# Optimization experiments

Hardware: AMD Instinct MI355X
Metric: run time of the kernel (lower is better)

## Reference

```python
import jax, jax.numpy as jnp
import numpy as np

E = 16          # num_experts
F_C = 2.0       # capacity factor
D = 1024        # embed_dim
I = 4 * D       # expert intermediate (mlp_ratio * embed_dim)
IS = 2 * D      # shared-expert intermediate (num_shared_experts * embed_dim)
B, S = 4, 1024


def setup_inputs() -> dict:
    key = jax.random.key(0)
    ks = jax.random.split(key, 8)
    w = 0.02
    return {
        "hidden_states": jax.random.normal(ks[0], (B, S, D), dtype=jnp.float32),
        "gate_w": jax.random.normal(ks[1], (E, D), dtype=jnp.float32) * w,
        "Wg": jax.random.normal(ks[2], (E, I, D), dtype=jnp.float32) * w,  # gate_proj per expert
        "Wu": jax.random.normal(ks[3], (E, I, D), dtype=jnp.float32) * w,  # up_proj per expert
        "Wd": jax.random.normal(ks[4], (E, D, I), dtype=jnp.float32) * w,  # down_proj per expert
        "Sg": jax.random.normal(ks[5], (IS, D), dtype=jnp.float32) * w,    # shared gate_proj
        "Su": jax.random.normal(ks[6], (IS, D), dtype=jnp.float32) * w,    # shared up_proj
        "Sd": jax.random.normal(ks[7], (D, IS), dtype=jnp.float32) * w,    # shared down_proj
    }


def reference(hidden_states, gate_w, Wg, Wu, Wd, Sg, Su, Sd):
    b, s, d = hidden_states.shape
    T = b * s
    C = int(T * F_C / E)  # expert capacity, static
    flat_x = hidden_states.reshape(T, d)

    # --- expert-choice gating ---
    logits = flat_x @ gate_w.T                      # (T, E)
    scores = jax.nn.softmax(logits, axis=-1).T      # (E, T)
    topk_weight, topk_idx = jax.lax.top_k(scores, C)  # (E, C)

    # --- gather tokens per expert ---
    xg = flat_x[topk_idx]                           # (E, C, d)

    # --- per-expert GELU-gated MLP (batched as grouped GEMMs) ---
    g = jnp.einsum('ecd,eid->eci', xg, Wg)          # (E, C, I)
    u = jnp.einsum('ecd,eid->eci', xg, Wu)          # (E, C, I)
    h = jax.nn.gelu(g, approximate=False) * u       # exact GELU matches nn.GELU()
    eo = jnp.einsum('eci,edi->ecd', h, Wd)          # (E, C, d)
    eo = eo * topk_weight[..., None]

    # --- weighted scatter-add back to tokens ---
    flat_out = jnp.zeros_like(flat_x).at[topk_idx.reshape(-1)].add(eo.reshape(-1, d))
    out = flat_out.reshape(b, s, d)

    # --- shared experts on all tokens ---
    sg = hidden_states @ Sg.T                       # (B, S, IS)
    su = hidden_states @ Su.T
    shared = (jax.nn.gelu(sg, approximate=False) * su) @ Sd.T  # (B, S, d)
    return out + shared
```

## Files before the change

kernel.cpp:

```cpp
#include <hip/hip_runtime.h>
#include <hip/hip_bf16.h>
#include <math.h>

#define NE   16
#define DDIM 1024
#define II   4096
#define ISD  2048
#define TT   4096
#define CAP  512

typedef __attribute__((ext_vector_type(8))) short short8;
typedef __attribute__((ext_vector_type(4))) float floatx4;

static __device__ __forceinline__ unsigned short f2b(float f){
  unsigned int x = __float_as_uint(f);
  return (unsigned short)((x + 0x7fffu + ((x >> 16) & 1u)) >> 16);
}

static __device__ __forceinline__ float gelu_exact(float x){
  return 0.5f * x * (1.0f + erff(x * 0.70710678118654752f));
}

#define ASYNC_COPY16(gptr, lptr)                                                    \
  __builtin_amdgcn_global_load_lds((const __attribute__((address_space(1))) void*)(gptr), \
                                   (__attribute__((address_space(3))) void*)(lptr), \
                                   16, 0, 0)

__global__ void gating_kernel(const float* __restrict__ x, const float* __restrict__ gw,
                              float* __restrict__ scores){
  const int wave = threadIdx.x >> 6, lane = threadIdx.x & 63;
  const int t = blockIdx.x * 4 + wave;
  const float* xp = x + (size_t)t * DDIM;
  float xr[16];
  #pragma unroll
  for (int i = 0; i < 16; i++) xr[i] = xp[i * 64 + lane];
  double logit[NE];
  #pragma unroll
  for (int e = 0; e < NE; e++){
    const float* g = gw + (size_t)e * DDIM;
    double s = 0.0;
    #pragma unroll
    for (int i = 0; i < 16; i++) s += (double)xr[i] * (double)g[i * 64 + lane];
    #pragma unroll
    for (int off = 32; off > 0; off >>= 1) s += __shfl_xor(s, off);
    logit[e] = s;
  }
  double m = logit[0];
  #pragma unroll
  for (int e = 1; e < NE; e++) m = fmax(m, logit[e]);
  double p[NE], sum = 0.0;
  #pragma unroll
  for (int e = 0; e < NE; e++){ p[e] = exp(logit[e] - m); sum += p[e]; }
  if (lane == 0){
    #pragma unroll
    for (int e = 0; e < NE; e++) scores[(size_t)e * TT + t] = (float)(p[e] / sum);
  }
}

__global__ void topk_kernel(const float* __restrict__ scores, int* __restrict__ cnt,
                            int* __restrict__ tidx, float* __restrict__ tw){
  const int e = blockIdx.y;
  __shared__ float s[TT];
  const float* se = scores + (size_t)e * TT;
  for (int i = threadIdx.x; i < TT; i += 256) s[i] = se[i];
  __syncthreads();
  const int t = blockIdx.x * 256 + threadIdx.x;
  const float ms = s[t];
  int r = 0;
  const float4* s4 = reinterpret_cast<const float4*>(s);
  for (int j = 0; j < TT / 4; j++){
    float4 v = s4[j];
    int b = j * 4;
    r += (v.x > ms) || (v.x == ms && (b + 0) < t);
    r += (v.y > ms) || (v.y == ms && (b + 1) < t);
    r += (v.z > ms) || (v.z == ms && (b + 2) < t);
    r += (v.w > ms) || (v.w == ms && (b + 3) < t);
  }
  if (r < CAP){
    int p = atomicAdd(&cnt[e], 1);
    tidx[e * CAP + p] = t;
    tw[e * CAP + p]   = ms;
  }
}

__global__ void cvt_bf16_kernel(const float* __restrict__ src, unsigned short* __restrict__ dst,
                                int n4){
  int i = blockIdx.x * 256 + threadIdx.x;
  const int stride = gridDim.x * 256;
  const float4* s = reinterpret_cast<const float4*>(src);
  ushort4* d = reinterpret_cast<ushort4*>(dst);
  for (; i < n4; i += stride){
    float4 v = s[i];
    ushort4 o; o.x = f2b(v.x); o.y = f2b(v.y); o.z = f2b(v.z); o.w = f2b(v.w);
    d[i] = o;
  }
}

__global__ void gather_b16_kernel(const unsigned short* __restrict__ xb,
                                  const int* __restrict__ tidx,
                                  unsigned short* __restrict__ Xg){
  const int ec = blockIdx.x;
  const int tok = tidx[ec];
  const ushort4* src = reinterpret_cast<const ushort4*>(xb + (size_t)tok * DDIM);
  ushort4* dst = reinterpret_cast<ushort4*>(Xg + (size_t)ec * DDIM);
  dst[threadIdx.x] = src[threadIdx.x];
}

__global__ void gather_kernel(const float* __restrict__ x, const int* __restrict__ tidx,
                              unsigned short* __restrict__ Xg){
  const int ec = blockIdx.x;
  const int tok = tidx[ec];
  const float4* src = reinterpret_cast<const float4*>(x + (size_t)tok * DDIM);
  ushort4* dst = reinterpret_cast<ushort4*>(Xg + (size_t)ec * DDIM);
  float4 v = src[threadIdx.x];
  ushort4 o; o.x = f2b(v.x); o.y = f2b(v.y); o.z = f2b(v.z); o.w = f2b(v.w);
  dst[threadIdx.x] = o;
}

__launch_bounds__(256, 2)
__global__ void gateup_bf16_kernel(const unsigned short* __restrict__ A,
                                   const unsigned short* __restrict__ Bg,
                                   const unsigned short* __restrict__ Bu,
                                   unsigned short* __restrict__ Hout,
                                   int M, int N, int K, long sA, long sB, long sH){
  __shared__ __align__(16) unsigned short As[128 * 32];
  __shared__ __align__(16) unsigned short Bgs[128 * 32];
  __shared__ __align__(16) unsigned short Bus[128 * 32];
  const int tid = threadIdx.x;
  const int z = blockIdx.z;
  A  += (size_t)z * sA;  Bg += (size_t)z * sB;  Bu += (size_t)z * sB;  Hout += (size_t)z * sH;
  const int bm = blockIdx.x * 128, bn = blockIdx.y * 128;
  const int lane = tid & 63, wave = tid >> 6;
  const int wr = wave >> 1, wc = wave & 1;
  const int fr = lane & 15, fq = lane >> 4;

  const int srow = tid >> 2;
  const int scol = (tid & 3) * 8;
  const unsigned short* gA = A  + (size_t)(bm + srow) * K + scol;
  const unsigned short* gG = Bg + (size_t)(bn + srow) * K + scol;
  const unsigned short* gU = Bu + (size_t)(bn + srow) * K + scol;
  const size_t half = (size_t)64 * K;
  unsigned short* lA = As  + tid * 8;
  unsigned short* lG = Bgs + tid * 8;
  unsigned short* lU = Bus + tid * 8;

  floatx4 accG[4][4], accU[4][4];
  const floatx4 z4 = {0.f, 0.f, 0.f, 0.f};
  #pragma unroll
  for (int m = 0; m < 4; m++)
    #pragma unroll
    for (int n = 0; n < 4; n++){ accG[m][n] = z4; accU[m][n] = z4; }

  for (int k0 = 0; k0 < K; k0 += 32){
    ASYNC_COPY16(gA + k0,        lA);
    ASYNC_COPY16(gA + half + k0, lA + 2048);
    ASYNC_COPY16(gG + k0,        lG);
    ASYNC_COPY16(gG + half + k0, lG + 2048);
    ASYNC_COPY16(gU + k0,        lU);
    ASYNC_COPY16(gU + half + k0, lU + 2048);
    __syncthreads();
    short8 aF[4], gF[4], uF[4];
    #pragma unroll
    for (int m = 0; m < 4; m++)
      aF[m] = *reinterpret_cast<const short8*>(&As[(wr * 64 + m * 16 + fr) * 32 + fq * 8]);
    #pragma unroll
    for (int n = 0; n < 4; n++){
      gF[n] = *reinterpret_cast<const short8*>(&Bgs[(wc * 64 + n * 16 + fr) * 32 + fq * 8]);
      uF[n] = *reinterpret_cast<const short8*>(&Bus[(wc * 64 + n * 16 + fr) * 32 + fq * 8]);
    }
    #pragma unroll
    for (int m = 0; m < 4; m++)
      #pragma unroll
      for (int n = 0; n < 4; n++){
        accG[m][n] = __builtin_amdgcn_mfma_f32_16x16x32_bf16(aF[m], gF[n], accG[m][n], 0, 0, 0);
        accU[m][n] = __builtin_amdgcn_mfma_f32_16x16x32_bf16(aF[m], uF[n], accU[m][n], 0, 0, 0);
      }
    __syncthreads();
  }
  #pragma unroll
  for (int m = 0; m < 4; m++)
    #pragma unroll
    for (int n = 0; n < 4; n++){
      const int col  = bn + wc * 64 + n * 16 + fr;
      const int row0 = bm + wr * 64 + m * 16 + fq * 4;
      #pragma unroll
      for (int i = 0; i < 4; i++){
        float g = accG[m][n][i], u = accU[m][n][i];
        Hout[(size_t)(row0 + i) * N + col] = f2b(gelu_exact(g) * u);
      }
    }
}

template<int ATOMIC>
__launch_bounds__(256, 2)
__global__ void down_bf16_kernel(const unsigned short* __restrict__ A,
                                 const unsigned short* __restrict__ B,
                                 float* __restrict__ out,
                                 const int* __restrict__ tidx, const float* __restrict__ tw,
                                 int M, int N, int K, long sA, long sB){
  __shared__ __align__(16) unsigned short As[128 * 32];
  __shared__ __align__(16) unsigned short Bs[128 * 32];
  const int tid = threadIdx.x;
  const int z = blockIdx.z;
  A += (size_t)z * sA;  B += (size_t)z * sB;
  const int bm = blockIdx.x * 128, bn = blockIdx.y * 128;
  const int lane = tid & 63, wave = tid >> 6;
  const int wr = wave >> 1, wc = wave & 1;
  const int fr = lane & 15, fq = lane >> 4;

  const int srow = tid >> 2;
  const int scol = (tid & 3) * 8;
  const unsigned short* gA = A + (size_t)(bm + srow) * K + scol;
  const unsigned short* gB = B + (size_t)(bn + srow) * K + scol;
  const size_t half = (size_t)64 * K;
  unsigned short* lA = As + tid * 8;
  unsigned short* lB = Bs + tid * 8;

  floatx4 acc[4][4];
  const floatx4 z4 = {0.f, 0.f, 0.f, 0.f};
  #pragma unroll
  for (int m = 0; m < 4; m++)
    #pragma unroll
    for (int n = 0; n < 4; n++) acc[m][n] = z4;

  for (int k0 = 0; k0 < K; k0 += 32){
    ASYNC_COPY16(gA + k0,        lA);
    ASYNC_COPY16(gA + half + k0, lA + 2048);
    ASYNC_COPY16(gB + k0,        lB);
    ASYNC_COPY16(gB + half + k0, lB + 2048);
    __syncthreads();
    short8 aF[4], bF[4];
    #pragma unroll
    for (int m = 0; m < 4; m++)
      aF[m] = *reinterpret_cast<const short8*>(&As[(wr * 64 + m * 16 + fr) * 32 + fq * 8]);
    #pragma unroll
    for (int n = 0; n < 4; n++)
      bF[n] = *reinterpret_cast<const short8*>(&Bs[(wc * 64 + n * 16 + fr) * 32 + fq * 8]);
    #pragma unroll
    for (int m = 0; m < 4; m++)
      #pragma unroll
      for (int n = 0; n < 4; n++)
        acc[m][n] = __builtin_amdgcn_mfma_f32_16x16x32_bf16(aF[m], bF[n], acc[m][n], 0, 0, 0);
    __syncthreads();
  }
  #pragma unroll
  for (int m = 0; m < 4; m++)
    #pragma unroll
    for (int n = 0; n < 4; n++){
      const int col  = bn + wc * 64 + n * 16 + fr;
      const int row0 = bm + wr * 64 + m * 16 + fq * 4;
      #pragma unroll
      for (int i = 0; i < 4; i++){
        float val = acc[m][n][i];
        if constexpr (ATOMIC){
          const int r = row0 + i;
          const int token = tidx[z * CAP + r];
          const float wgt = tw[z * CAP + r];
          atomicAdd(&out[(size_t)token * DDIM + col], val * wgt);
        } else {
          out[(size_t)(row0 + i) * N + col] = val;
        }
      }
    }
}

#define LDT 40
template<typename TA>
__launch_bounds__(256, 2)
__global__ void gateup_kernel(const TA* __restrict__ A, const float* __restrict__ Bg,
                              const float* __restrict__ Bu, unsigned short* __restrict__ H,
                              int M, int N, int K, long sA, long sB, long sH){
  __shared__ unsigned short As[128 * LDT];
  __shared__ unsigned short Bgs[128 * LDT];
  __shared__ unsigned short Bus[128 * LDT];
  const int tid = threadIdx.x;
  const int z = blockIdx.z;
  A  += (size_t)z * sA;  Bg += (size_t)z * sB;  Bu += (size_t)z * sB;  H += (size_t)z * sH;
  const int bm = blockIdx.x * 128, bn = blockIdx.y * 128;
  const int lane = tid & 63, wave = tid >> 6;
  const int wr = wave >> 1, wc = wave & 1;
  const int fr = lane & 15, fq = lane >> 4;

  floatx4 accG[4][4], accU[4][4];
  const floatx4 z4 = {0.f, 0.f, 0.f, 0.f};
  #pragma unroll
  for (int m = 0; m < 4; m++)
    #pragma unroll
    for (int n = 0; n < 4; n++){ accG[m][n] = z4; accU[m][n] = z4; }

  for (int k0 = 0; k0 < K; k0 += 32){
    #pragma unroll
    for (int p = 0; p < 4; p++){
      const int row = p * 32 + (tid >> 3);
      const int col = (tid & 7) * 4;
      if constexpr (__is_same(TA, float)){
        float4 v = *reinterpret_cast<const float4*>(A + (size_t)(bm + row) * K + k0 + col);
        ushort4 o; o.x = f2b(v.x); o.y = f2b(v.y); o.z = f2b(v.z); o.w = f2b(v.w);
        *reinterpret_cast<ushort4*>(&As[row * LDT + col]) = o;
      } else {
        *reinterpret_cast<ushort4*>(&As[row * LDT + col]) =
            *reinterpret_cast<const ushort4*>(A + (size_t)(bm + row) * K + k0 + col);
      }
      float4 vg = *reinterpret_cast<const float4*>(Bg + (size_t)(bn + row) * K + k0 + col);
      ushort4 og; og.x = f2b(vg.x); og.y = f2b(vg.y); og.z = f2b(vg.z); og.w = f2b(vg.w);
      *reinterpret_cast<ushort4*>(&Bgs[row * LDT + col]) = og;
      float4 vu = *reinterpret_cast<const float4*>(Bu + (size_t)(bn + row) * K + k0 + col);
      ushort4 ou; ou.x = f2b(vu.x); ou.y = f2b(vu.y); ou.z = f2b(vu.z); ou.w = f2b(vu.w);
      *reinterpret_cast<ushort4*>(&Bus[row * LDT + col]) = ou;
    }
    __syncthreads();
    short8 aF[4], gF[4], uF[4];
    #pragma unroll
    for (int m = 0; m < 4; m++)
      aF[m] = *reinterpret_cast<const short8*>(&As[(wr * 64 + m * 16 + fr) * LDT + fq * 8]);
    #pragma unroll
    for (int n = 0; n < 4; n++){
      gF[n] = *reinterpret_cast<const short8*>(&Bgs[(wc * 64 + n * 16 + fr) * LDT + fq * 8]);
      uF[n] = *reinterpret_cast<const short8*>(&Bus[(wc * 64 + n * 16 + fr) * LDT + fq * 8]);
    }
    #pragma unroll
    for (int m = 0; m < 4; m++)
      #pragma unroll
      for (int n = 0; n < 4; n++){
        accG[m][n] = __builtin_amdgcn_mfma_f32_16x16x32_bf16(aF[m], gF[n], accG[m][n], 0, 0, 0);
        accU[m][n] = __builtin_amdgcn_mfma_f32_16x16x32_bf16(aF[m], uF[n], accU[m][n], 0, 0, 0);
      }
    __syncthreads();
  }
  #pragma unroll
  for (int m = 0; m < 4; m++)
    #pragma unroll
    for (int n = 0; n < 4; n++){
      const int col  = bn + wc * 64 + n * 16 + fr;
      const int row0 = bm + wr * 64 + m * 16 + fq * 4;
      #pragma unroll
      for (int i = 0; i < 4; i++){
        float g = accG[m][n][i], u = accU[m][n][i];
        H[(size_t)(row0 + i) * N + col] = f2b(gelu_exact(g) * u);
      }
    }
}

template<int ATOMIC>
__launch_bounds__(256, 2)
__global__ void down_kernel(const unsigned short* __restrict__ A, const float* __restrict__ B,
                            float* __restrict__ out, const int* __restrict__ tidx,
                            const float* __restrict__ tw,
                            int M, int N, int K, long sA, long sB){
  __shared__ unsigned short As[128 * LDT];
  __shared__ unsigned short Bs[128 * LDT];
  const int tid = threadIdx.x;
  const int z = blockIdx.z;
  A += (size_t)z * sA;  B += (size_t)z * sB;
  const int bm = blockIdx.x * 128, bn = blockIdx.y * 128;
  const int lane = tid & 63, wave = tid >> 6;
  const int wr = wave >> 1, wc = wave & 1;
  const int fr = lane & 15, fq = lane >> 4;

  floatx4 acc[4][4];
  const floatx4 z4 = {0.f, 0.f, 0.f, 0.f};
  #pragma unroll
  for (int m = 0; m < 4; m++)
    #pragma unroll
    for (int n = 0; n < 4; n++) acc[m][n] = z4;

  for (int k0 = 0; k0 < K; k0 += 32){
    #pragma unroll
    for (int p = 0; p < 4; p++){
      const int row = p * 32 + (tid >> 3);
      const int col = (tid & 7) * 4;
      *reinterpret_cast<ushort4*>(&As[row * LDT + col]) =
          *reinterpret_cast<const ushort4*>(A + (size_t)(bm + row) * K + k0 + col);
      float4 v = *reinterpret_cast<const float4*>(B + (size_t)(bn + row) * K + k0 + col);
      ushort4 o; o.x = f2b(v.x); o.y = f2b(v.y); o.z = f2b(v.z); o.w = f2b(v.w);
      *reinterpret_cast<ushort4*>(&Bs[row * LDT + col]) = o;
    }
    __syncthreads();
    short8 aF[4], bF[4];
    #pragma unroll
    for (int m = 0; m < 4; m++)
      aF[m] = *reinterpret_cast<const short8*>(&As[(wr * 64 + m * 16 + fr) * LDT + fq * 8]);
    #pragma unroll
    for (int n = 0; n < 4; n++)
      bF[n] = *reinterpret_cast<const short8*>(&Bs[(wc * 64 + n * 16 + fr) * LDT + fq * 8]);
    #pragma unroll
    for (int m = 0; m < 4; m++)
      #pragma unroll
      for (int n = 0; n < 4; n++)
        acc[m][n] = __builtin_amdgcn_mfma_f32_16x16x32_bf16(aF[m], bF[n], acc[m][n], 0, 0, 0);
    __syncthreads();
  }
  #pragma unroll
  for (int m = 0; m < 4; m++)
    #pragma unroll
    for (int n = 0; n < 4; n++){
      const int col  = bn + wc * 64 + n * 16 + fr;
      const int row0 = bm + wr * 64 + m * 16 + fq * 4;
      #pragma unroll
      for (int i = 0; i < 4; i++){
        float val = acc[m][n][i];
        if constexpr (ATOMIC){
          const int r = row0 + i;
          const int token = tidx[z * CAP + r];
          const float wgt = tw[z * CAP + r];
          atomicAdd(&out[(size_t)token * DDIM + col], val * wgt);
        } else {
          out[(size_t)(row0 + i) * N + col] = val;
        }
      }
    }
}

extern "C" void kernel_launch(void* const* d_in, const int* in_sizes, int n_in,
                              void* d_out, int out_size, void* d_ws, size_t ws_size,
                              hipStream_t stream){
  const float* x  = (const float*)d_in[0];
  const float* gw = (const float*)d_in[1];
  const float* Wg = (const float*)d_in[2];
  const float* Wu = (const float*)d_in[3];
  const float* Wd = (const float*)d_in[4];
  const float* Sg = (const float*)d_in[5];
  const float* Su = (const float*)d_in[6];
  const float* Sd = (const float*)d_in[7];
  float* out = (float*)d_out;

  char* w = (char*)d_ws;
  float* scores        = (float*)w;           w += (size_t)NE * TT * 4;
  int*   cnt           = (int*)w;             w += 256;
  int*   tidx          = (int*)w;             w += (size_t)NE * CAP * 4;
  float* tw            = (float*)w;           w += (size_t)NE * CAP * 4;
  unsigned short* Xg   = (unsigned short*)w;  w += (size_t)NE * CAP * DDIM * 2;
  unsigned short* H    = (unsigned short*)w;  w += (size_t)NE * CAP * II * 2;
  unsigned short* Hs   = (unsigned short*)w;  w += (size_t)TT * ISD * 2;

  const size_t base_used = (size_t)(w - (char*)d_ws);
  const size_t need_extra = (size_t)TT * DDIM * 2
                          + (size_t)NE * II * DDIM * 2 * 2
                          + (size_t)NE * DDIM * II * 2
                          + (size_t)ISD * DDIM * 2 * 2
                          + (size_t)DDIM * ISD * 2;
  const bool fast = (base_used + need_extra) <= ws_size;

  hipMemsetAsync(cnt, 0, NE * sizeof(int), stream);
  gating_kernel<<<TT / 4, 256, 0, stream>>>(x, gw, scores);
  topk_kernel<<<dim3(TT / 256, NE), 256, 0, stream>>>(scores, cnt, tidx, tw);

  if (fast){
    unsigned short* xb  = (unsigned short*)w;  w += (size_t)TT * DDIM * 2;
    unsigned short* bWg = (unsigned short*)w;  w += (size_t)NE * II * DDIM * 2;
    unsigned short* bWu = (unsigned short*)w;  w += (size_t)NE * II * DDIM * 2;
    unsigned short* bWd = (unsigned short*)w;  w += (size_t)NE * DDIM * II * 2;
    unsigned short* bSg = (unsigned short*)w;  w += (size_t)ISD * DDIM * 2;
    unsigned short* bSu = (unsigned short*)w;  w += (size_t)ISD * DDIM * 2;
    unsigned short* bSd = (unsigned short*)w;  w += (size_t)DDIM * ISD * 2;

    cvt_bf16_kernel<<<1024, 256, 0, stream>>>(x,  xb,  TT * DDIM / 4);
    cvt_bf16_kernel<<<2048, 256, 0, stream>>>(Wg, bWg, NE * II * DDIM / 4);
    cvt_bf16_kernel<<<2048, 256, 0, stream>>>(Wu, bWu, NE * II * DDIM / 4);
    cvt_bf16_kernel<<<2048, 256, 0, stream>>>(Wd, bWd, NE * DDIM * II / 4);
    cvt_bf16_kernel<<<512, 256, 0, stream>>>(Sg, bSg, ISD * DDIM / 4);
    cvt_bf16_kernel<<<512, 256, 0, stream>>>(Su, bSu, ISD * DDIM / 4);
    cvt_bf16_kernel<<<512, 256, 0, stream>>>(Sd, bSd, DDIM * ISD / 4);

    gather_b16_kernel<<<NE * CAP, 256, 0, stream>>>(xb, tidx, Xg);

    gateup_bf16_kernel<<<dim3(TT / 128, ISD / 128, 1), 256, 0, stream>>>(
        xb, bSg, bSu, Hs, TT, ISD, DDIM, 0, 0, 0);
    down_bf16_kernel<0><<<dim3(TT / 128, DDIM / 128, 1), 256, 0, stream>>>(
        Hs, bSd, out, nullptr, nullptr, TT, DDIM, ISD, 0, 0);

    gateup_bf16_kernel<<<dim3(CAP / 128, II / 128, NE), 256, 0, stream>>>(
        Xg, bWg, bWu, H, CAP, II, DDIM, (long)CAP * DDIM, (long)II * DDIM, (long)CAP * II);
    down_bf16_kernel<1><<<dim3(CAP / 128, DDIM / 128, NE), 256, 0, stream>>>(
        H, bWd, out, tidx, tw, CAP, DDIM, II, (long)CAP * II, (long)DDIM * II);
  } else {
    gather_kernel<<<NE * CAP, 256, 0, stream>>>(x, tidx, Xg);

    gateup_kernel<float><<<dim3(TT / 128, ISD / 128, 1), 256, 0, stream>>>(
        x, Sg, Su, Hs, TT, ISD, DDIM, 0, 0, 0);
    down_kernel<0><<<dim3(TT / 128, DDIM / 128, 1), 256, 0, stream>>>(
        Hs, Sd, out, nullptr, nullptr, TT, DDIM, ISD, 0, 0);

    gateup_kernel<unsigned short><<<dim3(CAP / 128, II / 128, NE), 256, 0, stream>>>(
        Xg, Wg, Wu, H, CAP, II, DDIM, (long)CAP * DDIM, (long)II * DDIM, (long)CAP * II);
    down_kernel<1><<<dim3(CAP / 128, DDIM / 128, NE), 256, 0, stream>>>(
        H, Wd, out, tidx, tw, CAP, DDIM, II, (long)CAP * II, (long)DDIM * II);
  }
}
```

Before: 1.380 ms.

## Double-buffer GEMM tiles, fuse fp32→bf16 down-weight conversion, flatten grid with XCD swizzle

```diff
diff --git a/kernel.cpp b/kernel.cpp
--- a/kernel.cpp
+++ b/kernel.cpp
@@ -25,6 +25,12 @@
   __builtin_amdgcn_global_load_lds((const __attribute__((address_space(1))) void*)(gptr), \
                                    (__attribute__((address_space(3))) void*)(lptr), \
                                    16, 0, 0)
+
+static __device__ __forceinline__ int xcd_swizzle(int lid, int nblk){
+  if (nblk & 7) return lid;
+  const int cpx = nblk >> 3;
+  return (lid & 7) * cpx + (lid >> 3);
+}
 
 __global__ void gating_kernel(const float* __restrict__ x, const float* __restrict__ gw,
                               float* __restrict__ scores){
@@ -118,31 +124,28 @@
 }
 
 __launch_bounds__(256, 2)
-__global__ void gateup_bf16_kernel(const unsigned short* __restrict__ A,
-                                   const unsigned short* __restrict__ Bg,
-                                   const unsigned short* __restrict__ Bu,
-                                   unsigned short* __restrict__ Hout,
-                                   int M, int N, int K, long sA, long sB, long sH){
-  __shared__ __align__(16) unsigned short As[128 * 32];
-  __shared__ __align__(16) unsigned short Bgs[128 * 32];
-  __shared__ __align__(16) unsigned short Bus[128 * 32];
+__global__ void gateup2_kernel(const unsigned short* __restrict__ A,
+                               const unsigned short* __restrict__ Bg,
+                               const unsigned short* __restrict__ Bu,
+                               unsigned short* __restrict__ Hout,
+                               int M, int N, int K, long sB, int nm){
+  __shared__ __align__(16) unsigned short As[2][128 * 32];
+  __shared__ __align__(16) unsigned short Bgs[2][128 * 32];
+  __shared__ __align__(16) unsigned short Bus[2][128 * 32];
   const int tid = threadIdx.x;
-  const int z = blockIdx.z;
-  A  += (size_t)z * sA;  Bg += (size_t)z * sB;  Bu += (size_t)z * sB;  Hout += (size_t)z * sH;
-  const int bm = blockIdx.x * 128, bn = blockIdx.y * 128;
+  const int swz = xcd_swizzle(blockIdx.x, gridDim.x);
+  const int mt = swz % nm, ntile = swz / nm;
+  const int bm = mt * 128, bn = ntile * 128;
+  Bg += (size_t)(mt >> 2) * sB;
+  Bu += (size_t)(mt >> 2) * sB;
   const int lane = tid & 63, wave = tid >> 6;
   const int wr = wave >> 1, wc = wave & 1;
   const int fr = lane & 15, fq = lane >> 4;
 
-  const int srow = tid >> 2;
-  const int scol = (tid & 3) * 8;
-  const unsigned short* gA = A  + (size_t)(bm + srow) * K + scol;
-  const unsigned short* gG = Bg + (size_t)(bn + srow) * K + scol;
-  const unsigned short* gU = Bu + (size_t)(bn + srow) * K + scol;
+  const unsigned short* gA = A  + (size_t)(bm + (tid >> 2)) * K + (tid & 3) * 8;
+  const unsigned short* gG = Bg + (size_t)(bn + (tid >> 2)) * K + (tid & 3) * 8;
+  const unsigned short* gU = Bu + (size_t)(bn + (tid >> 2)) * K + (tid & 3) * 8;
   const size_t half = (size_t)64 * K;
-  unsigned short* lA = As  + tid * 8;
-  unsigned short* lG = Bgs + tid * 8;
-  unsigned short* lU = Bus + tid * 8;
 
   floatx4 accG[4][4], accU[4][4];
   const floatx4 z4 = {0.f, 0.f, 0.f, 0.f};
@@ -151,22 +154,28 @@
     #pragma unroll
     for (int n = 0; n < 4; n++){ accG[m][n] = z4; accU[m][n] = z4; }
 
+  auto stage = [&](int b, int k0){
+    ASYNC_COPY16(gA + k0,        &As[b][tid * 8]);
+    ASYNC_COPY16(gA + half + k0, &As[b][tid * 8 + 2048]);
+    ASYNC_COPY16(gG + k0,        &Bgs[b][tid * 8]);
+    ASYNC_COPY16(gG + half + k0, &Bgs[b][tid * 8 + 2048]);
+    ASYNC_COPY16(gU + k0,        &Bus[b][tid * 8]);
+    ASYNC_COPY16(gU + half + k0, &Bus[b][tid * 8 + 2048]);
+  };
+
+  stage(0, 0);
+  __syncthreads();
+  int buf = 0;
   for (int k0 = 0; k0 < K; k0 += 32){
-    ASYNC_COPY16(gA + k0,        lA);
-    ASYNC_COPY16(gA + half + k0, lA + 2048);
-    ASYNC_COPY16(gG + k0,        lG);
-    ASYNC_COPY16(gG + half + k0, lG + 2048);
-    ASYNC_COPY16(gU + k0,        lU);
-    ASYNC_COPY16(gU + half + k0, lU + 2048);
-    __syncthreads();
+    if (k0 + 32 < K) stage(buf ^ 1, k0 + 32);
     short8 aF[4], gF[4], uF[4];
     #pragma unroll
     for (int m = 0; m < 4; m++)
-      aF[m] = *reinterpret_cast<const short8*>(&As[(wr * 64 + m * 16 + fr) * 32 + fq * 8]);
+      aF[m] = *reinterpret_cast<const short8*>(&As[buf][(wr * 64 + m * 16 + fr) * 32 + fq * 8]);
     #pragma unroll
     for (int n = 0; n < 4; n++){
-      gF[n] = *reinterpret_cast<const short8*>(&Bgs[(wc * 64 + n * 16 + fr) * 32 + fq * 8]);
-      uF[n] = *reinterpret_cast<const short8*>(&Bus[(wc * 64 + n * 16 + fr) * 32 + fq * 8]);
+      gF[n] = *reinterpret_cast<const short8*>(&Bgs[buf][(wc * 64 + n * 16 + fr) * 32 + fq * 8]);
+      uF[n] = *reinterpret_cast<const short8*>(&Bus[buf][(wc * 64 + n * 16 + fr) * 32 + fq * 8]);
     }
     #pragma unroll
     for (int m = 0; m < 4; m++)
@@ -176,6 +185,7 @@
         accU[m][n] = __builtin_amdgcn_mfma_f32_16x16x32_bf16(aF[m], uF[n], accU[m][n], 0, 0, 0);
       }
     __syncthreads();
+    buf ^= 1;
   }
   #pragma unroll
   for (int m = 0; m < 4; m++)
@@ -193,28 +203,24 @@
 
 template<int ATOMIC>
 __launch_bounds__(256, 2)
-__global__ void down_bf16_kernel(const unsigned short* __restrict__ A,
-                                 const unsigned short* __restrict__ B,
-                                 float* __restrict__ out,
-                                 const int* __restrict__ tidx, const float* __restrict__ tw,
-                                 int M, int N, int K, long sA, long sB){
-  __shared__ __align__(16) unsigned short As[128 * 32];
-  __shared__ __align__(16) unsigned short Bs[128 * 32];
+__global__ void down2_kernel(const unsigned short* __restrict__ A, const float* __restrict__ B,
+                             float* __restrict__ out, const int* __restrict__ tidx,
+                             const float* __restrict__ tw,
+                             int M, int N, int K, long sB, int nm){
+  __shared__ __align__(16) unsigned short As[2][128 * 32];
+  __shared__ __align__(16) unsigned short Bs[2][128 * 32];
   const int tid = threadIdx.x;
-  const int z = blockIdx.z;
-  A += (size_t)z * sA;  B += (size_t)z * sB;
-  const int bm = blockIdx.x * 128, bn = blockIdx.y * 128;
+  const int swz = xcd_swizzle(blockIdx.x, gridDim.x);
+  const int mt = swz % nm, ntile = swz / nm;
+  const int bm = mt * 128, bn = ntile * 128;
+  B += (size_t)(mt >> 2) * sB;
   const int lane = tid & 63, wave = tid >> 6;
   const int wr = wave >> 1, wc = wave & 1;
   const int fr = lane & 15, fq = lane >> 4;
 
-  const int srow = tid >> 2;
-  const int scol = (tid & 3) * 8;
-  const unsigned short* gA = A + (size_t)(bm + srow) * K + scol;
-  const unsigned short* gB = B + (size_t)(bn + srow) * K + scol;
+  const unsigned short* gA = A + (size_t)(bm + (tid >> 2)) * K + (tid & 3) * 8;
+  const float* gB = B + (size_t)bn * K;
   const size_t half = (size_t)64 * K;
-  unsigned short* lA = As + tid * 8;
-  unsigned short* lB = Bs + tid * 8;
 
   floatx4 acc[4][4];
   const floatx4 z4 = {0.f, 0.f, 0.f, 0.f};
@@ -223,25 +229,40 @@
     #pragma unroll
     for (int n = 0; n < 4; n++) acc[m][n] = z4;
 
+  auto stageA = [&](int b, int k0){
+    ASYNC_COPY16(gA + k0,        &As[b][tid * 8]);
+    ASYNC_COPY16(gA + half + k0, &As[b][tid * 8 + 2048]);
+  };
+  auto stageB = [&](int b, int k0){
+    #pragma unroll
+    for (int p = 0; p < 4; p++){
+      const int row = p * 32 + (tid >> 3);
+      const int col = (tid & 7) * 4;
+      float4 v = *reinterpret_cast<const float4*>(gB + (size_t)row * K + k0 + col);
+      ushort4 o; o.x = f2b(v.x); o.y = f2b(v.y); o.z = f2b(v.z); o.w = f2b(v.w);
+      *reinterpret_cast<ushort4*>(&Bs[b][row * 32 + col]) = o;
+    }
+  };
+
+  stageA(0, 0); stageB(0, 0);
+  __syncthreads();
+  int buf = 0;
   for (int k0 = 0; k0 < K; k0 += 32){
-    ASYNC_COPY16(gA + k0,        lA);
-    ASYNC_COPY16(gA + half + k0, lA + 2048);
-    ASYNC_COPY16(gB + k0,        lB);
-    ASYNC_COPY16(gB + half + k0, lB + 2048);
-    __syncthreads();
+    if (k0 + 32 < K){ stageA(buf ^ 1, k0 + 32); stageB(buf ^ 1, k0 + 32); }
     short8 aF[4], bF[4];
     #pragma unroll
     for (int m = 0; m < 4; m++)
-      aF[m] = *reinterpret_cast<const short8*>(&As[(wr * 64 + m * 16 + fr) * 32 + fq * 8]);
+      aF[m] = *reinterpret_cast<const short8*>(&As[buf][(wr * 64 + m * 16 + fr) * 32 + fq * 8]);
     #pragma unroll
     for (int n = 0; n < 4; n++)
-      bF[n] = *reinterpret_cast<const short8*>(&Bs[(wc * 64 + n * 16 + fr) * 32 + fq * 8]);
+      bF[n] = *reinterpret_cast<const short8*>(&Bs[buf][(wc * 64 + n * 16 + fr) * 32 + fq * 8]);
     #pragma unroll
     for (int m = 0; m < 4; m++)
       #pragma unroll
       for (int n = 0; n < 4; n++)
         acc[m][n] = __builtin_amdgcn_mfma_f32_16x16x32_bf16(aF[m], bF[n], acc[m][n], 0, 0, 0);
     __syncthreads();
+    buf ^= 1;
   }
   #pragma unroll
   for (int m = 0; m < 4; m++)
@@ -254,8 +275,8 @@
         float val = acc[m][n][i];
         if constexpr (ATOMIC){
           const int r = row0 + i;
-          const int token = tidx[z * CAP + r];
-          const float wgt = tw[z * CAP + r];
+          const int token = tidx[r];
+          const float wgt = tw[r];
           atomicAdd(&out[(size_t)token * DDIM + col], val * wgt);
         } else {
           out[(size_t)(row0 + i) * N + col] = val;
@@ -436,9 +457,7 @@
   const size_t base_used = (size_t)(w - (char*)d_ws);
   const size_t need_extra = (size_t)TT * DDIM * 2
                           + (size_t)NE * II * DDIM * 2 * 2
-                          + (size_t)NE * DDIM * II * 2
-                          + (size_t)ISD * DDIM * 2 * 2
-                          + (size_t)DDIM * ISD * 2;
+                          + (size_t)ISD * DDIM * 2 * 2;
   const bool fast = (base_used + need_extra) <= ws_size;
 
   hipMemsetAsync(cnt, 0, NE * sizeof(int), stream);
@@ -449,30 +468,26 @@
     unsigned short* xb  = (unsigned short*)w;  w += (size_t)TT * DDIM * 2;
     unsigned short* bWg = (unsigned short*)w;  w += (size_t)NE * II * DDIM * 2;
     unsigned short* bWu = (unsigned short*)w;  w += (size_t)NE * II * DDIM * 2;
-    unsigned short* bWd = (unsigned short*)w;  w += (size_t)NE * DDIM * II * 2;
     unsigned short* bSg = (unsigned short*)w;  w += (size_t)ISD * DDIM * 2;
     unsigned short* bSu = (unsigned short*)w;  w += (size_t)ISD * DDIM * 2;
-    unsigned short* bSd = (unsigned short*)w;  w += (size_t)DDIM * ISD * 2;
 
     cvt_bf16_kernel<<<1024, 256, 0, stream>>>(x,  xb,  TT * DDIM / 4);
     cvt_bf16_kernel<<<2048, 256, 0, stream>>>(Wg, bWg, NE * II * DDIM / 4);
     cvt_bf16_kernel<<<2048, 256, 0, stream>>>(Wu, bWu, NE * II * DDIM / 4);
-    cvt_bf16_kernel<<<2048, 256, 0, stream>>>(Wd, bWd, NE * DDIM * II / 4);
     cvt_bf16_kernel<<<512, 256, 0, stream>>>(Sg, bSg, ISD * DDIM / 4);
     cvt_bf16_kernel<<<512, 256, 0, stream>>>(Su, bSu, ISD * DDIM / 4);
-    cvt_bf16_kernel<<<512, 256, 0, stream>>>(Sd, bSd, DDIM * ISD / 4);
 
     gather_b16_kernel<<<NE * CAP, 256, 0, stream>>>(xb, tidx, Xg);
 
-    gateup_bf16_kernel<<<dim3(TT / 128, ISD / 128, 1), 256, 0, stream>>>(
-        xb, bSg, bSu, Hs, TT, ISD, DDIM, 0, 0, 0);
-    down_bf16_kernel<0><<<dim3(TT / 128, DDIM / 128, 1), 256, 0, stream>>>(
-        Hs, bSd, out, nullptr, nullptr, TT, DDIM, ISD, 0, 0);
-
-    gateup_bf16_kernel<<<dim3(CAP / 128, II / 128, NE), 256, 0, stream>>>(
-        Xg, bWg, bWu, H, CAP, II, DDIM, (long)CAP * DDIM, (long)II * DDIM, (long)CAP * II);
-    down_bf16_kernel<1><<<dim3(CAP / 128, DDIM / 128, NE), 256, 0, stream>>>(
-        H, bWd, out, tidx, tw, CAP, DDIM, II, (long)CAP * II, (long)DDIM * II);
+    gateup2_kernel<<<(TT / 128) * (ISD / 128), 256, 0, stream>>>(
+        xb, bSg, bSu, Hs, TT, ISD, DDIM, 0L, TT / 128);
+    down2_kernel<0><<<(TT / 128) * (DDIM / 128), 256, 0, stream>>>(
+        Hs, Sd, out, nullptr, nullptr, TT, DDIM, ISD, 0L, TT / 128);
+
+    gateup2_kernel<<<(NE * CAP / 128) * (II / 128), 256, 0, stream>>>(
+        Xg, bWg, bWu, H, NE * CAP, II, DDIM, (long)II * DDIM, NE * CAP / 128);
+    down2_kernel<1><<<(NE * CAP / 128) * (DDIM / 128), 256, 0, stream>>>(
+        H, Wd, out, tidx, tw, NE * CAP, DDIM, II, (long)DDIM * II, NE * CAP / 128);
   } else {
     gather_kernel<<<NE * CAP, 256, 0, stream>>>(x, tidx, Xg);
 
```

Result: faster. 1.337 ms (-3.1%).
